# Kernel optimization log

Hardware: AMD Instinct MI355X
Metric: run time of the kernel (lower is better)

## Reference

```python
import jax, jax.numpy as jnp
import numpy as np

TEMP = 0.05
ALPHA = 1.0
ETA = 10
M = 8192
N = 2048
H = 1024


def l2norm(x, eps=1e-12):
    n = jnp.linalg.norm(x, axis=-1, keepdims=True)
    return x / jnp.maximum(n, eps)


def setup_inputs() -> dict:
    key = jax.random.key(0)
    k1, k2, k3 = jax.random.split(key, 3)
    q = jax.random.normal(k1, (N, H), dtype=jnp.float32)
    k = jax.random.normal(k2, (N, H), dtype=jnp.float32)
    B_init = jnp.zeros((M, H), dtype=jnp.float32)  # normalized zeros stay zeros
    noise = jax.random.normal(k3, (ETA, M, H), dtype=jnp.float32)
    return {"q": q, "k": k, "B_init": B_init, "noise": noise}


def _em_loop(B, q, noise):
    # Langevin-EM memory-bank update (runs under no_grad in the original).
    def step(B, inp):
        i, Q = inp  # i: 0-based iteration index, Q: [M,H] noise
        L = B @ q.T                                   # [M, N]
        L_norm = jax.nn.softmax(L / TEMP, axis=-1)    # [M, N]
        delta_B1 = L_norm @ q / N - jnp.mean(L_norm * L, axis=1, keepdims=True) * B
        delta_B = B @ (B.T @ delta_B1) / M + B        # [M, H]
        t = i + 1.0
        B_new = (B
                 + ALPHA * 0.5 / t * delta_B
                 + ALPHA * 0.5 / t * delta_B1
                 + jnp.sqrt(2.0 * ALPHA / t) * Q)
        return l2norm(B_new), None

    steps = jnp.arange(ETA, dtype=jnp.float32)
    B, _ = jax.lax.scan(step, B, (steps, noise))
    return B


def reference(q, k, B_init, noise):
    q = l2norm(q)
    k = l2norm(k)
    B = jax.lax.stop_gradient(_em_loop(B_init, q, noise))  # no_grad block
    logit_neg = q @ B.T / TEMP                              # [N, M]
    cos_sim = jnp.einsum('bh,bh->b', q, k)[:, None] / TEMP  # [N, 1]
    return jnp.concatenate([cos_sim, logit_neg], axis=-1)   # [N, 1+M]
```

## Files before the change

### kernel.cpp

```cpp
#include <hip/hip_runtime.h>
#include <math.h>

#define TEMP_INV 20.0f
#define MM 8192
#define NN 2048
#define HH 1024
#define ETA_IT 10
#define SLD 72

typedef float4 f4;
typedef unsigned short u16;
using short8 = __attribute__((ext_vector_type(8))) short;
using f32x4  = __attribute__((ext_vector_type(4))) float;

__device__ __forceinline__ u16 f2bf(float x) {
  union { float f; unsigned u; } v; v.f = x;
  unsigned r = v.u + 0x7FFFu + ((v.u >> 16) & 1u);
  return (u16)(r >> 16);
}
__device__ __forceinline__ float bf2f(u16 h) {
  union { unsigned u; float f; } v; v.u = ((unsigned)h) << 16;
  return v.f;
}

__device__ __forceinline__ float waveReduceSum(float v) {
#pragma unroll
  for (int off = 32; off > 0; off >>= 1) v += __shfl_xor(v, off, 64);
  return v;
}
__device__ __forceinline__ float waveReduceMax(float v) {
#pragma unroll
  for (int off = 32; off > 0; off >>= 1) v = fmaxf(v, __shfl_xor(v, off, 64));
  return v;
}
__device__ __forceinline__ float blockReduceSum(float v, float* tmp) {
  int tid = threadIdx.x;
  v = waveReduceSum(v);
  if ((tid & 63) == 0) tmp[tid >> 6] = v;
  __syncthreads();
  float r = tmp[0] + tmp[1] + tmp[2] + tmp[3];
  __syncthreads();
  return r;
}
__device__ __forceinline__ float blockReduceMax(float v, float* tmp) {
  int tid = threadIdx.x;
  v = waveReduceMax(v);
  if ((tid & 63) == 0) tmp[tid >> 6] = v;
  __syncthreads();
  float r = fmaxf(fmaxf(tmp[0], tmp[1]), fmaxf(tmp[2], tmp[3]));
  __syncthreads();
  return r;
}

__global__ __launch_bounds__(256) void rownorm_split_k(const float* __restrict__ src,
                                                       float* __restrict__ dst,
                                                       u16* __restrict__ dhi,
                                                       u16* __restrict__ dlo) {
  __shared__ float tmp[4];
  int row = blockIdx.x;
  int tid = threadIdx.x;
  f4 v = *(const f4*)(src + (size_t)row * HH + tid * 4);
  float ss = v.x * v.x + v.y * v.y + v.z * v.z + v.w * v.w;
  ss = blockReduceSum(ss, tmp);
  float inv = 1.0f / fmaxf(sqrtf(ss), 1e-12f);
  v.x *= inv; v.y *= inv; v.z *= inv; v.w *= inv;
  *(f4*)(dst + (size_t)row * HH + tid * 4) = v;
  union { u16 u[4]; uint2 q; } H, L;
  float vv[4] = {v.x, v.y, v.z, v.w};
#pragma unroll
  for (int j = 0; j < 4; ++j) {
    H.u[j] = f2bf(vv[j]);
    L.u[j] = f2bf(vv[j] - bf2f(H.u[j]));
  }
  *(uint2*)(dhi + (size_t)row * HH + tid * 4) = H.q;
  *(uint2*)(dlo + (size_t)row * HH + tid * 4) = L.q;
}

__global__ __launch_bounds__(256) void colmean_k(const float* __restrict__ qn,
                                                 float* __restrict__ qcm) {
  int h = blockIdx.x * 256 + threadIdx.x;
  float s = 0.f;
  for (int n = 0; n < NN; ++n) s += qn[(size_t)n * HH + h];
  qcm[h] = s * (0.5f / ((float)NN * (float)NN));
}
__global__ __launch_bounds__(256) void init0_k(const float* __restrict__ qcm,
                                               const float* __restrict__ noise,
                                               float* __restrict__ Bm,
                                               u16* __restrict__ bhi, u16* __restrict__ blo) {
  __shared__ float tmp[4];
  int m = blockIdx.x;
  int tid = threadIdx.x;
  const float c2 = 1.41421356237309515f;
  f4 qv = *(const f4*)(qcm + tid * 4);
  f4 nv = *(const f4*)(noise + (size_t)m * HH + tid * 4);
  f4 v = make_float4(qv.x + c2 * nv.x, qv.y + c2 * nv.y, qv.z + c2 * nv.z, qv.w + c2 * nv.w);
  float ss = v.x * v.x + v.y * v.y + v.z * v.z + v.w * v.w;
  ss = blockReduceSum(ss, tmp);
  float inv = 1.0f / fmaxf(sqrtf(ss), 1e-12f);
  v.x *= inv; v.y *= inv; v.z *= inv; v.w *= inv;
  *(f4*)(Bm + (size_t)m * HH + tid * 4) = v;
  union { u16 u[4]; uint2 q; } H, L;
  float vv[4] = {v.x, v.y, v.z, v.w};
#pragma unroll
  for (int j = 0; j < 4; ++j) {
    H.u[j] = f2bf(vv[j]);
    L.u[j] = f2bf(vv[j] - bf2f(H.u[j]));
  }
  *(uint2*)(bhi + (size_t)m * HH + tid * 4) = H.q;
  *(uint2*)(blo + (size_t)m * HH + tid * 4) = L.q;
}

__global__ __launch_bounds__(256) void transpose_split_k(const float* __restrict__ src,
                                                         u16* __restrict__ hiT,
                                                         u16* __restrict__ loT,
                                                         int R, int C) {
  __shared__ float T[32][33];
  int c0 = blockIdx.x * 32, r0 = blockIdx.y * 32;
  int t = threadIdx.x;
  int j = t & 31, i4 = t >> 5;
#pragma unroll
  for (int ii = 0; ii < 4; ++ii) {
    int i = i4 * 4 + ii;
    T[i][j] = src[(size_t)(r0 + i) * C + c0 + j];
  }
  __syncthreads();
#pragma unroll
  for (int ii = 0; ii < 4; ++ii) {
    int i = i4 * 4 + ii;
    float v = T[j][i];
    u16 h = f2bf(v);
    size_t o = (size_t)(c0 + i) * R + r0 + j;
    hiT[o] = h;
    loT[o] = f2bf(v - bf2f(h));
  }
}

__global__ __launch_bounds__(256) void cos_k(const float* __restrict__ qn,
                                             const float* __restrict__ k,
                                             float* __restrict__ out) {
  __shared__ float tmp[4];
  int row = blockIdx.x;
  int tid = threadIdx.x;
  f4 a = *(const f4*)(qn + (size_t)row * HH + tid * 4);
  f4 b = *(const f4*)(k + (size_t)row * HH + tid * 4);
  float dot = a.x * b.x + a.y * b.y + a.z * b.z + a.w * b.w;
  float kk = b.x * b.x + b.y * b.y + b.z * b.z + b.w * b.w;
  dot = blockReduceSum(dot, tmp);
  kk = blockReduceSum(kk, tmp);
  if (tid == 0)
    out[(size_t)row * (MM + 1)] = dot / fmaxf(sqrtf(kk), 1e-12f) * TEMP_INV;
}

__global__ __launch_bounds__(256) void rowstats_k(const float* __restrict__ L,
                                                  u16* __restrict__ Ehi, u16* __restrict__ Elo,
                                                  float* __restrict__ sA,
                                                  float* __restrict__ sB) {
  __shared__ float tmp[4];
  int m = blockIdx.x;
  int tid = threadIdx.x;
  const float* row = L + (size_t)m * NN;
  f4 v0 = *(const f4*)(row + tid * 8);
  f4 v1 = *(const f4*)(row + tid * 8 + 4);
  float vals[8] = {v0.x, v0.y, v0.z, v0.w, v1.x, v1.y, v1.z, v1.w};
  float mx = vals[0];
#pragma unroll
  for (int j = 1; j < 8; ++j) mx = fmaxf(mx, vals[j]);
  mx = blockReduceMax(mx, tmp);
  float e[8], es = 0.f, els = 0.f;
#pragma unroll
  for (int j = 0; j < 8; ++j) {
    e[j] = expf((vals[j] - mx) * TEMP_INV);
    es += e[j];
    els += e[j] * vals[j];
  }
  es = blockReduceSum(es, tmp);
  els = blockReduceSum(els, tmp);
  union { u16 u[8]; uint4 q; } H, Lo;
#pragma unroll
  for (int j = 0; j < 8; ++j) {
    H.u[j] = f2bf(e[j]);
    Lo.u[j] = f2bf(e[j] - bf2f(H.u[j]));
  }
  *(uint4*)(Ehi + (size_t)m * NN + tid * 8) = H.q;
  *(uint4*)(Elo + (size_t)m * NN + tid * 8) = Lo.q;
  if (tid == 0) {
    float inv = 1.0f / (es * (float)NN);
    sA[m] = inv;
    sB[m] = els * inv;
  }
}

__device__ __forceinline__ void gemm_core(const u16* __restrict__ Ahi, const u16* __restrict__ Alo,
                                          int lda,
                                          const u16* __restrict__ Bhi, const u16* __restrict__ Blo,
                                          int ldb, int K, int m0, int n0, int tid,
                                          u16* As, u16* Bs, f32x4 acc[4][4]) {
  const int lane = tid & 63, w = tid >> 6;
  const int wr = w >> 1, wc = w & 1;
  const int fr = lane & 15, kg = lane >> 4;
  const int nt = 3 * K / 64;
  for (int kt = 0; kt < nt; ++kt) {
    const int reg = (kt * 64) / K;
    const int k0 = kt * 64 - reg * K;
    const u16* asrc = (reg < 2) ? Ahi : Alo;
    const u16* bsrc = (reg == 1) ? Blo : Bhi;
#pragma unroll
    for (int rep = 0; rep < 4; ++rep) {
      int slot = tid + rep * 256;
      int x = slot >> 3, c8 = (slot & 7) << 3;
      *(uint4*)(As + x * SLD + c8) = *(const uint4*)(asrc + (size_t)(m0 + x) * lda + k0 + c8);
      *(uint4*)(Bs + x * SLD + c8) = *(const uint4*)(bsrc + (size_t)(n0 + x) * ldb + k0 + c8);
    }
    __syncthreads();
#pragma unroll
    for (int ks = 0; ks < 64; ks += 32) {
      short8 a[4], b[4];
#pragma unroll
      for (int mi = 0; mi < 4; ++mi)
        a[mi] = *(const short8*)(As + (wr * 64 + mi * 16 + fr) * SLD + ks + kg * 8);
#pragma unroll
      for (int ni = 0; ni < 4; ++ni)
        b[ni] = *(const short8*)(Bs + (wc * 64 + ni * 16 + fr) * SLD + ks + kg * 8);
#pragma unroll
      for (int mi = 0; mi < 4; ++mi)
#pragma unroll
        for (int ni = 0; ni < 4; ++ni)
          acc[mi][ni] = __builtin_amdgcn_mfma_f32_16x16x32_bf16(a[mi], b[ni], acc[mi][ni], 0, 0, 0);
    }
    __syncthreads();
  }
}

#define GEMM_PROLOGUE()                                     \
  __shared__ u16 As[128 * SLD], Bs[128 * SLD];              \
  int tid = threadIdx.x;                                    \
  f32x4 acc[4][4];                                          \
  {                                                         \
    f32x4 z = {0.f, 0.f, 0.f, 0.f};                         \
    _Pragma("unroll") for (int i = 0; i < 4; ++i)           \
        _Pragma("unroll") for (int j = 0; j < 4; ++j) acc[i][j] = z; \
  }                                                         \
  const int lane = tid & 63, wv = tid >> 6;                 \
  const int wr = wv >> 1, wc = wv & 1;                      \
  const int fr = lane & 15, kg = lane >> 4;


__global__ __launch_bounds__(256) void gemm_L_k(const u16* __restrict__ Ahi, const u16* __restrict__ Alo,
                                                const u16* __restrict__ Bhi, const u16* __restrict__ Blo,
                                                float* __restrict__ L) {
  GEMM_PROLOGUE();
  int n0 = blockIdx.x * 128, m0 = blockIdx.y * 128;
  gemm_core(Ahi, Alo, HH, Bhi, Blo, HH, HH, m0, n0, tid, As, Bs, acc);
#pragma unroll
  for (int mi = 0; mi < 4; ++mi)
#pragma unroll
    for (int r = 0; r < 4; ++r) {
      int m = m0 + wr * 64 + mi * 16 + kg * 4 + r;
      float* dst = L + (size_t)m * NN + n0 + wc * 64 + fr;
#pragma unroll
      for (int ni = 0; ni < 4; ++ni) dst[ni * 16] = acc[mi][ni][r];
    }
}

__global__ __launch_bounds__(256) void gemm_dB1_k(const u16* __restrict__ Ahi, const u16* __restrict__ Alo,
                                                  const u16* __restrict__ Bhi, const u16* __restrict__ Blo,
                                                  const float* __restrict__ Bm,
                                                  const float* __restrict__ sA,
                                                  const float* __restrict__ sB,
                                                  float* __restrict__ dB1) {
  GEMM_PROLOGUE();
  int n0 = blockIdx.x * 128, m0 = blockIdx.y * 128;
  gemm_core(Ahi, Alo, NN, Bhi, Blo, NN, NN, m0, n0, tid, As, Bs, acc);
#pragma unroll
  for (int mi = 0; mi < 4; ++mi)
#pragma unroll
    for (int r = 0; r < 4; ++r) {
      int m = m0 + wr * 64 + mi * 16 + kg * 4 + r;
      float a = sA[m], bc = sB[m];
      size_t base = (size_t)m * HH + n0 + wc * 64 + fr;
#pragma unroll
      for (int ni = 0; ni < 4; ++ni)
        dB1[base + ni * 16] = acc[mi][ni][r] * a - bc * Bm[base + ni * 16];
    }
}

__global__ __launch_bounds__(256) void gemm_G_k(const u16* __restrict__ Ahi, const u16* __restrict__ Alo,
                                                const u16* __restrict__ Bhi, const u16* __restrict__ Blo,
                                                float* __restrict__ Gp) {
  GEMM_PROLOGUE();
  int n0 = blockIdx.x * 128, m0 = blockIdx.y * 128;
  int kbase = blockIdx.z * (MM / 8);
  gemm_core(Ahi + kbase, Alo + kbase, MM, Bhi + kbase, Blo + kbase, MM, MM / 8, m0, n0, tid, As, Bs, acc);
  float* dst0 = Gp + (size_t)blockIdx.z * HH * HH;
#pragma unroll
  for (int mi = 0; mi < 4; ++mi)
#pragma unroll
    for (int r = 0; r < 4; ++r) {
      int h1 = m0 + wr * 64 + mi * 16 + kg * 4 + r;
      float* dst = dst0 + (size_t)h1 * HH + n0 + wc * 64 + fr;
#pragma unroll
      for (int ni = 0; ni < 4; ++ni) dst[ni * 16] = acc[mi][ni][r];
    }
}

__global__ __launch_bounds__(256) void reduceG_k(const float* __restrict__ Gp,
                                                 float* __restrict__ G) {
  size_t i = ((size_t)blockIdx.x * 256 + threadIdx.x) * 4;
  f4 s = make_float4(0.f, 0.f, 0.f, 0.f);
#pragma unroll
  for (int sl = 0; sl < 8; ++sl) {
    f4 v = *(const f4*)(Gp + (size_t)sl * HH * HH + i);
    s.x += v.x; s.y += v.y; s.z += v.z; s.w += v.w;
  }
  const float invM = 1.0f / (float)MM;
  s.x *= invM; s.y *= invM; s.z *= invM; s.w *= invM;
  *(f4*)(G + i) = s;
}

__global__ __launch_bounds__(256) void gemm_upd_k(const u16* __restrict__ Ahi, const u16* __restrict__ Alo,
                                                  const u16* __restrict__ Bhi, const u16* __restrict__ Blo,
                                                  const float* __restrict__ Bm,
                                                  const float* __restrict__ noise,
                                                  float* __restrict__ dB1, float c1, float c2) {
  GEMM_PROLOGUE();
  int n0 = blockIdx.x * 128, m0 = blockIdx.y * 128;
  gemm_core(Ahi, Alo, HH, Bhi, Blo, HH, HH, m0, n0, tid, As, Bs, acc);
  const float c1p = 1.0f + c1;
#pragma unroll
  for (int mi = 0; mi < 4; ++mi)
#pragma unroll
    for (int r = 0; r < 4; ++r) {
      int m = m0 + wr * 64 + mi * 16 + kg * 4 + r;
      size_t base = (size_t)m * HH + n0 + wc * 64 + fr;
#pragma unroll
      for (int ni = 0; ni < 4; ++ni) {
        size_t o = base + ni * 16;
        dB1[o] = c1 * acc[mi][ni][r] + c1p * Bm[o] + c1 * dB1[o] + c2 * noise[o];
      }
    }
}

__global__ __launch_bounds__(256) void gemm_out_k(const u16* __restrict__ Ahi, const u16* __restrict__ Alo,
                                                  const u16* __restrict__ Bhi, const u16* __restrict__ Blo,
                                                  float* __restrict__ out) {
  GEMM_PROLOGUE();
  int n0 = blockIdx.x * 128, m0 = blockIdx.y * 128;
  gemm_core(Ahi, Alo, HH, Bhi, Blo, HH, HH, m0, n0, tid, As, Bs, acc);
#pragma unroll
  for (int mi = 0; mi < 4; ++mi)
#pragma unroll
    for (int r = 0; r < 4; ++r) {
      int n = m0 + wr * 64 + mi * 16 + kg * 4 + r;
      float* dst = out + (size_t)n * (MM + 1) + 1 + n0 + wc * 64 + fr;
#pragma unroll
      for (int ni = 0; ni < 4; ++ni) dst[ni * 16] = acc[mi][ni][r] * TEMP_INV;
    }
}

extern "C" void kernel_launch(void* const* d_in, const int* in_sizes, int n_in, void* d_out,
                              int out_size, void* d_ws, size_t ws_size, hipStream_t stream) {
  (void)in_sizes; (void)n_in; (void)out_size; (void)ws_size;
  const float* q = (const float*)d_in[0];
  const float* k = (const float*)d_in[1];
  const float* noise = (const float*)d_in[3];
  float* out = (float*)d_out;

  char* w = (char*)d_ws;
  size_t off = 0;
  auto alloc = [&](size_t bytes) -> void* {
    void* p = w + off;
    off = (off + bytes + 255) & ~(size_t)255;
    return p;
  };
  float* qn     = (float*)alloc((size_t)NN * HH * 4);
  u16*   qn_hi  = (u16*)  alloc((size_t)NN * HH * 2);
  u16*   qn_lo  = (u16*)  alloc((size_t)NN * HH * 2);
  u16*   qnT_hi = (u16*)  alloc((size_t)HH * NN * 2);
  u16*   qnT_lo = (u16*)  alloc((size_t)HH * NN * 2);
  float* Bm     = (float*)alloc((size_t)MM * HH * 4);
  u16*   Bm_hi  = (u16*)  alloc((size_t)MM * HH * 2);
  u16*   Bm_lo  = (u16*)  alloc((size_t)MM * HH * 2);
  u16*   BmT_hi = (u16*)  alloc((size_t)HH * MM * 2);
  u16*   BmT_lo = (u16*)  alloc((size_t)HH * MM * 2);
  float* dB1    = (float*)alloc((size_t)MM * HH * 4);
  u16*   E_hi   = (u16*)  alloc((size_t)MM * NN * 2);
  u16*   E_lo   = (u16*)  alloc((size_t)MM * NN * 2);
  float* Gp     = (float*)E_hi;
  u16*   dB1T_hi = (u16*)E_lo;
  u16*   dB1T_lo = dB1T_hi + (size_t)HH * MM;
  float* G      = (float*)alloc((size_t)HH * HH * 4);
  u16*   GT_hi  = (u16*)  alloc((size_t)HH * HH * 2);
  u16*   GT_lo  = (u16*)  alloc((size_t)HH * HH * 2);
  float* sA     = (float*)alloc(MM * 4);
  float* sB     = (float*)alloc(MM * 4);
  float* qcm    = (float*)alloc(HH * 4);
  float* L = out;

  rownorm_split_k<<<NN, 256, 0, stream>>>(q, qn, qn_hi, qn_lo);
  transpose_split_k<<<dim3(HH / 32, NN / 32), 256, 0, stream>>>(qn, qnT_hi, qnT_lo, NN, HH);
  colmean_k<<<HH / 256, 256, 0, stream>>>(qn, qcm);
  init0_k<<<MM, 256, 0, stream>>>(qcm, noise, Bm, Bm_hi, Bm_lo);
  transpose_split_k<<<dim3(HH / 32, MM / 32), 256, 0, stream>>>(Bm, BmT_hi, BmT_lo, MM, HH);

  for (int it = 1; it < ETA_IT; ++it) {
    float t = (float)it + 1.0f;
    float c1 = 0.5f / t;
    float c2 = sqrtf(2.0f / t);
    gemm_L_k<<<dim3(NN / 128, MM / 128), 256, 0, stream>>>(Bm_hi, Bm_lo, qn_hi, qn_lo, L);
    rowstats_k<<<MM, 256, 0, stream>>>(L, E_hi, E_lo, sA, sB);
    gemm_dB1_k<<<dim3(HH / 128, MM / 128), 256, 0, stream>>>(E_hi, E_lo, qnT_hi, qnT_lo, Bm, sA, sB, dB1);
    transpose_split_k<<<dim3(HH / 32, MM / 32), 256, 0, stream>>>(dB1, dB1T_hi, dB1T_lo, MM, HH);
    gemm_G_k<<<dim3(HH / 128, HH / 128, 8), 256, 0, stream>>>(BmT_hi, BmT_lo, dB1T_hi, dB1T_lo, Gp);
    reduceG_k<<<(HH * HH / 4) / 256, 256, 0, stream>>>(Gp, G);
    transpose_split_k<<<dim3(HH / 32, HH / 32), 256, 0, stream>>>(G, GT_hi, GT_lo, HH, HH);
    gemm_upd_k<<<dim3(HH / 128, MM / 128), 256, 0, stream>>>(
        Bm_hi, Bm_lo, GT_hi, GT_lo, Bm, noise + (size_t)it * MM * HH, dB1, c1, c2);
    rownorm_split_k<<<MM, 256, 0, stream>>>(dB1, Bm, Bm_hi, Bm_lo);
    transpose_split_k<<<dim3(HH / 32, MM / 32), 256, 0, stream>>>(Bm, BmT_hi, BmT_lo, MM, HH);
  }

  cos_k<<<NN, 256, 0, stream>>>(qn, k, out);
  gemm_out_k<<<dim3(MM / 128, NN / 128), 256, 0, stream>>>(qn_hi, qn_lo, Bm_hi, Bm_lo, out);
}
```

Baseline: 5.417 ms.

## Load GEMM tiles directly to LDS with XOR swizzle and XCD-aware block remap

Tile loads in the shared GEMM core now use global_load_lds, which writes global memory straight into LDS without going through registers. The padded LDS stride is replaced by an XOR swizzle on 64-wide rows to avoid bank conflicts. Each GEMM kernel also remaps its block index so that neighbouring tiles are placed on the same XCD, which is meant to improve L2 reuse. The main risk is correctness of the swizzle against the global_load_lds write pattern, and the remap assumes the tile count divides by 8.

```diff
diff --git a/kernel.cpp b/kernel.cpp
--- a/kernel.cpp
+++ b/kernel.cpp
@@ -6,7 +6,6 @@
 #define NN 2048
 #define HH 1024
 #define ETA_IT 10
-#define SLD 72
 
 typedef float4 f4;
 typedef unsigned short u16;
@@ -21,6 +20,21 @@
 __device__ __forceinline__ float bf2f(u16 h) {
   union { unsigned u; float f; } v; v.u = ((unsigned)h) << 16;
   return v.f;
+}
+
+__device__ __forceinline__ void gload16(const u16* __restrict__ g, u16* l) {
+  __builtin_amdgcn_global_load_lds((const __attribute__((address_space(1))) void*)g,
+                                   (__attribute__((address_space(3))) void*)l, 16, 0, 0);
+}
+
+__device__ __forceinline__ void xcd_swz(int& bx, int& by) {
+  int gx = gridDim.x;
+  int nwg = gx * gridDim.y;
+  int wg = blockIdx.y * gx + blockIdx.x;
+  int cpx = nwg >> 3;
+  int s = (wg & 7) * cpx + (wg >> 3);
+  bx = s % gx;
+  by = s / gx;
 }
 
 __device__ __forceinline__ float waveReduceSum(float v) {
@@ -195,9 +209,12 @@
                                           const u16* __restrict__ Bhi, const u16* __restrict__ Blo,
                                           int ldb, int K, int m0, int n0, int tid,
                                           u16* As, u16* Bs, f32x4 acc[4][4]) {
-  const int lane = tid & 63, w = tid >> 6;
-  const int wr = w >> 1, wc = w & 1;
+  const int lane = tid & 63, wv = tid >> 6;
+  const int wr = wv >> 1, wc = wv & 1;
   const int fr = lane & 15, kg = lane >> 4;
+  const int lrow = lane >> 3;
+  const int sblk = ((lane & 7) ^ lrow) << 3;
+  const int xoff = (kg ^ (fr & 7)) << 3;
   const int nt = 3 * K / 64;
   for (int kt = 0; kt < nt; ++kt) {
     const int reg = (kt * 64) / K;
@@ -205,11 +222,10 @@
     const u16* asrc = (reg < 2) ? Ahi : Alo;
     const u16* bsrc = (reg == 1) ? Blo : Bhi;
 #pragma unroll
-    for (int rep = 0; rep < 4; ++rep) {
-      int slot = tid + rep * 256;
-      int x = slot >> 3, c8 = (slot & 7) << 3;
-      *(uint4*)(As + x * SLD + c8) = *(const uint4*)(asrc + (size_t)(m0 + x) * lda + k0 + c8);
-      *(uint4*)(Bs + x * SLD + c8) = *(const uint4*)(bsrc + (size_t)(n0 + x) * ldb + k0 + c8);
+    for (int c4 = 0; c4 < 4; ++c4) {
+      const int c = wv * 4 + c4;
+      gload16(asrc + (size_t)(m0 + c * 8 + lrow) * lda + k0 + sblk, As + c * 512);
+      gload16(bsrc + (size_t)(n0 + c * 8 + lrow) * ldb + k0 + sblk, Bs + c * 512);
     }
     __syncthreads();
 #pragma unroll
@@ -217,10 +233,10 @@
       short8 a[4], b[4];
 #pragma unroll
       for (int mi = 0; mi < 4; ++mi)
-        a[mi] = *(const short8*)(As + (wr * 64 + mi * 16 + fr) * SLD + ks + kg * 8);
+        a[mi] = *(const short8*)(As + (wr * 64 + mi * 16 + fr) * 64 + (ks ^ xoff));
 #pragma unroll
       for (int ni = 0; ni < 4; ++ni)
-        b[ni] = *(const short8*)(Bs + (wc * 64 + ni * 16 + fr) * SLD + ks + kg * 8);
+        b[ni] = *(const short8*)(Bs + (wc * 64 + ni * 16 + fr) * 64 + (ks ^ xoff));
 #pragma unroll
       for (int mi = 0; mi < 4; ++mi)
 #pragma unroll
@@ -232,7 +248,7 @@
 }
 
 #define GEMM_PROLOGUE()                                     \
-  __shared__ u16 As[128 * SLD], Bs[128 * SLD];              \
+  __shared__ u16 As[128 * 64], Bs[128 * 64];                \
   int tid = threadIdx.x;                                    \
   f32x4 acc[4][4];                                          \
   {                                                         \
@@ -249,7 +265,8 @@
                                                 const u16* __restrict__ Bhi, const u16* __restrict__ Blo,
                                                 float* __restrict__ L) {
   GEMM_PROLOGUE();
-  int n0 = blockIdx.x * 128, m0 = blockIdx.y * 128;
+  int bx, by; xcd_swz(bx, by);
+  int n0 = bx * 128, m0 = by * 128;
   gemm_core(Ahi, Alo, HH, Bhi, Blo, HH, HH, m0, n0, tid, As, Bs, acc);
 #pragma unroll
   for (int mi = 0; mi < 4; ++mi)
@@ -269,7 +286,8 @@
                                                   const float* __restrict__ sB,
                                                   float* __restrict__ dB1) {
   GEMM_PROLOGUE();
-  int n0 = blockIdx.x * 128, m0 = blockIdx.y * 128;
+  int bx, by; xcd_swz(bx, by);
+  int n0 = bx * 128, m0 = by * 128;
   gemm_core(Ahi, Alo, NN, Bhi, Blo, NN, NN, m0, n0, tid, As, Bs, acc);
 #pragma unroll
   for (int mi = 0; mi < 4; ++mi)
@@ -288,7 +306,8 @@
                                                 const u16* __restrict__ Bhi, const u16* __restrict__ Blo,
                                                 float* __restrict__ Gp) {
   GEMM_PROLOGUE();
-  int n0 = blockIdx.x * 128, m0 = blockIdx.y * 128;
+  int bx, by; xcd_swz(bx, by);
+  int n0 = bx * 128, m0 = by * 128;
   int kbase = blockIdx.z * (MM / 8);
   gemm_core(Ahi + kbase, Alo + kbase, MM, Bhi + kbase, Blo + kbase, MM, MM / 8, m0, n0, tid, As, Bs, acc);
   float* dst0 = Gp + (size_t)blockIdx.z * HH * HH;
@@ -323,7 +342,8 @@
                                                   const float* __restrict__ noise,
                                                   float* __restrict__ dB1, float c1, float c2) {
   GEMM_PROLOGUE();
-  int n0 = blockIdx.x * 128, m0 = blockIdx.y * 128;
+  int bx, by; xcd_swz(bx, by);
+  int n0 = bx * 128, m0 = by * 128;
   gemm_core(Ahi, Alo, HH, Bhi, Blo, HH, HH, m0, n0, tid, As, Bs, acc);
   const float c1p = 1.0f + c1;
 #pragma unroll
@@ -344,7 +364,8 @@
                                                   const u16* __restrict__ Bhi, const u16* __restrict__ Blo,
                                                   float* __restrict__ out) {
   GEMM_PROLOGUE();
-  int n0 = blockIdx.x * 128, m0 = blockIdx.y * 128;
+  int bx, by; xcd_swz(bx, by);
+  int n0 = bx * 128, m0 = by * 128;
   gemm_core(Ahi, Alo, HH, Bhi, Blo, HH, HH, m0, n0, tid, As, Bs, acc);
 #pragma unroll
   for (int mi = 0; mi < 4; ++mi)
```

New measurement: 5.177 ms. 4.4% less time.
